# Performance work log

Measured on AMD Instinct MI355X. Metric: run time of the kernel, lower is better.

## Reference

```python
import jax, jax.numpy as jnp
import numpy as np

P, K, C = 16, 256, 3          # patches, boxes per patch, classes
PATCH = 1024                   # patch size (px)
SIZE_FACTOR = 1.0
IOU_T = 0.55                   # wbf_iou_thresh
PRE = P * K                    # pre_wbf_detections = 4096
POST = 1000                    # max_detections


def setup_inputs() -> dict:
    key = jax.random.key(0)
    k1, k2, k3, k4, k5, k6 = jax.random.split(key, 6)
    # realistic xyxy boxes inside a 1024px patch, 8..56 px wide
    cx = jax.random.uniform(k1, (P, K)) * (PATCH - 64)
    cy = jax.random.uniform(k2, (P, K)) * (PATCH - 64)
    w = jax.random.uniform(k3, (P, K)) * 48.0 + 8.0
    h = jax.random.uniform(k4, (P, K)) * 48.0 + 8.0
    b4 = jnp.stack([cx, cy, cx + w, cy + h], axis=-1)          # [P,K,4]
    scores = jax.random.uniform(k5, (P, K, 1))                  # (0,1)
    labels = jax.random.randint(k6, (P, K, 1), 0, C).astype(jnp.float32)
    boxes = jnp.concatenate([b4, scores, labels], axis=-1)      # [P,K,6]
    stride = float(int(PATCH * 0.8))
    grid = jnp.arange(4, dtype=jnp.float32) * stride
    ox = jnp.tile(grid, 4)
    oy = jnp.repeat(grid, 4)
    offsets = jnp.stack([ox, oy], axis=-1)                      # [P,2] (xmin,ymin)
    return {"boxes": boxes, "offsets": offsets}


def _wbf(dets):
    """Greedy class-aware weighted boxes fusion.

    dets: [N,6] = (x1,y1,x2,y2,score,label). Sequential scan: each box joins
    the first existing cluster of the SAME class with IoU(merged_box)>IOU_T,
    else opens a new cluster. Class-aware matching inside one scan is
    math-equivalent to the original per-class loops (clusters never mix
    classes; within-class order is preserved; output is score-sorted anyway).
    """
    N = dets.shape[0]
    init = (
        jnp.zeros((N, 4), jnp.float32),   # mbox: current merged box per slot
        jnp.zeros((N, 4), jnp.float32),   # wsum: sum(score*box)
        jnp.zeros((N,), jnp.float32),     # ssum: sum(score)
        jnp.zeros((N,), jnp.float32),     # cnt:  members per cluster
        jnp.full((N,), -1.0, jnp.float32),# cls:  cluster class id
        jnp.array(0, jnp.int32),          # num:  clusters opened so far
    )

    def step(carry, row):
        mbox, wsum, ssum, cnt, cls, num = carry
        box, score, label = row[:4], row[4], row[5]
        # IoU of `box` against every cluster slot (vectorized)
        xx1 = jnp.maximum(mbox[:, 0], box[0])
        yy1 = jnp.maximum(mbox[:, 1], box[1])
        xx2 = jnp.minimum(mbox[:, 2], box[2])
        yy2 = jnp.minimum(mbox[:, 3], box[3])
        inter = jnp.clip(xx2 - xx1, 0.0) * jnp.clip(yy2 - yy1, 0.0)
        area_a = (box[2] - box[0]) * (box[3] - box[1])
        area_b = (mbox[:, 2] - mbox[:, 0]) * (mbox[:, 3] - mbox[:, 1])
        union = area_a + area_b - inter
        iou = jnp.where(union > 0.0, inter / union, 0.0)
        match = (cnt > 0) & (cls == label) & (iou > IOU_T)
        has = jnp.any(match)
        idx = jnp.where(has, jnp.argmax(match).astype(jnp.int32), num)
        wsum = wsum.at[idx].add(score * box)
        ssum = ssum.at[idx].add(score)
        cnt = cnt.at[idx].add(1.0)
        mbox = mbox.at[idx].set(wsum[idx] / ssum[idx])
        cls = cls.at[idx].set(label)
        num = num + jnp.where(has, 0, 1).astype(jnp.int32)
        return (mbox, wsum, ssum, cnt, cls, num), None

    (mbox, wsum, ssum, cnt, cls, num), _ = jax.lax.scan(step, init, dets)
    valid = cnt > 0.0
    scores = jnp.where(valid, ssum / jnp.maximum(cnt, 1.0), 0.0)  # mean score
    return mbox, scores, cls, valid


def reference(boxes, offsets):
    # PatchMerger: shift boxes into global coords, rescale by size_factor
    off4 = jnp.concatenate([offsets, offsets], axis=-1)[:, None, :]  # [P,1,4]
    b4 = (boxes[..., :4] + off4) / SIZE_FACTOR                       # [P,K,4]
    dets = jnp.concatenate([b4, boxes[..., 4:]], axis=-1).reshape(-1, 6)[:PRE]
    # WBF clustering
    mbox, scores, cls, valid = _wbf(dets)
    # sort by score desc, keep top POST; pad rows zeroed
    sort_key = jnp.where(valid, scores, -1.0)
    topv, topi = jax.lax.top_k(sort_key, POST)
    out = jnp.concatenate([mbox, scores[:, None], cls[:, None]], axis=-1)[topi]
    out = jnp.where((topv >= 0.0)[:, None], out, 0.0)
    return out  # [POST, 6]
```

## Files before the change

### kernel.cpp

```cpp
#include <hip/hip_runtime.h>

#define N 4096
#define NT 1024
#define BATCH 64
#define KCAND 8
#define IOU_THR 0.55f
#define INF 0x7fffffff
#define NBINS 14
#define NBKT 42
#define BCAP 320

__device__ float4 g_wsum[N];

__device__ __forceinline__ float rl_f(float v, int lane) {
  return __int_as_float(__builtin_amdgcn_readlane(__float_as_int(v), lane));
}
__device__ __forceinline__ int rl_i(int v, int lane) {
  return __builtin_amdgcn_readlane(v, lane);
}

__global__ __launch_bounds__(NT) void wbf_kernel(
    const float* __restrict__ boxes,
    const float* __restrict__ offs,
    float* __restrict__ out)
{
  __shared__ float4 s_mbox[N];
  __shared__ float  s_ssum[N];
  __shared__ unsigned short s_cc[N];
  __shared__ unsigned short s_bkt[NBKT][BCAP];
  __shared__ int s_bktlen[NBKT];
  __shared__ unsigned long long s_dirty[64];
  __shared__ uint4 s_cand4[BATCH];
  __shared__ int   s_ccnt[BATCH];
  __shared__ float s_batch[BATCH][6];
  __shared__ unsigned s_bgate[BATCH];
  __shared__ unsigned long long s_pm[BATCH];
  __shared__ int s_min[2];
  __shared__ int s_num, s_resume, s_ovf;

  const int tid = threadIdx.x;

  if (tid < 64) s_dirty[tid] = 0ull;
  if (tid < NBKT) s_bktlen[tid] = 0;
  if (tid == 0) { s_num = 0; s_resume = BATCH; s_ovf = 0; s_min[0] = INF; s_min[1] = INF; }

  for (int t0 = 0; t0 < N; t0 += BATCH) {
    if (tid < BATCH * 6) {
      int b = tid / 6, f = tid % 6;
      int gi = t0 + b;
      float v = boxes[(size_t)gi * 6 + f];
      if (f < 4) v += offs[((gi >> 8) << 1) + (f & 1)];
      s_batch[b][f] = v;
    } else if (tid < BATCH * 7) {
      s_ccnt[tid - BATCH * 6] = 0;
    } else if (tid < BATCH * 8) {
      s_pm[tid - BATCH * 7] = 0ull;
    }
    __syncthreads();

    int nm0 = s_num;
    if (tid < BATCH) {
      int qx = (int)s_batch[tid][0];
      int qy = (int)s_batch[tid][1];
      int lb = (int)s_batch[tid][5];
      s_bgate[tid] = ((unsigned)((lb << 12) | qx) << 16) | (unsigned)qy;
    }
    __syncthreads();

    int use_linear = s_ovf;
    if (!use_linear) {
      int b = tid >> 4, sl = tid & 15;
      float qx1 = s_batch[b][0], qy1 = s_batch[b][1];
      float qx2 = s_batch[b][2], qy2 = s_batch[b][3];
      int cls = (int)s_batch[b][5];
      float aA = (qx2 - qx1) * (qy2 - qy1);
      int bb = ((int)qx1) >> 8;
      int jlo = bb > 0 ? bb - 1 : 0;
      int jhi = bb < NBINS - 1 ? bb + 1 : NBINS - 1;
      for (int j = jlo; j <= jhi; ++j) {
        int bk = cls * NBINS + j;
        int len = s_bktlen[bk]; if (len > BCAP) len = BCAP;
        for (int e = sl; e < len; e += 16) {
          int c = (int)s_bkt[bk][e];
          float4 m = s_mbox[c];
          if (fabsf(m.x - qx1) < 60.0f && fabsf(m.y - qy1) < 60.0f) {
            float xx1 = fmaxf(m.x, qx1), yy1 = fmaxf(m.y, qy1);
            float xx2 = fminf(m.z, qx2), yy2 = fminf(m.w, qy2);
            float iw = fmaxf(xx2 - xx1, 0.0f), ih = fmaxf(yy2 - yy1, 0.0f);
            float inter = iw * ih;
            float aB = (m.z - m.x) * (m.w - m.y);
            float uni = aA + aB - inter;
            if (uni > 0.0f && inter / uni > IOU_THR) {
              int pos = atomicAdd(&s_ccnt[b], 1);
              if (pos < KCAND) ((unsigned short*)&s_cand4[b])[pos] = (unsigned short)c;
            }
          }
        }
      }
    } else {
      for (int c = tid; c < nm0; c += NT) {
        float4 m = s_mbox[c];
        int mcls = (int)(s_cc[c] >> 14);
        float aB = (m.z - m.x) * (m.w - m.y);
        for (int b2 = 0; b2 < BATCH; ++b2) {
          float qx1 = s_batch[b2][0], qy1 = s_batch[b2][1];
          if (fabsf(m.x - qx1) < 60.0f && fabsf(m.y - qy1) < 60.0f &&
              mcls == (int)s_batch[b2][5]) {
            float qx2 = s_batch[b2][2], qy2 = s_batch[b2][3];
            float xx1 = fmaxf(m.x, qx1), yy1 = fmaxf(m.y, qy1);
            float xx2 = fminf(m.z, qx2), yy2 = fminf(m.w, qy2);
            float iw = fmaxf(xx2 - xx1, 0.0f), ih = fmaxf(yy2 - yy1, 0.0f);
            float inter = iw * ih;
            float aA = (qx2 - qx1) * (qy2 - qy1);
            float uni = aA + aB - inter;
            if (uni > 0.0f && inter / uni > IOU_THR) {
              int pos = atomicAdd(&s_ccnt[b2], 1);
              if (pos < KCAND) ((unsigned short*)&s_cand4[b2])[pos] = (unsigned short)c;
            }
          }
        }
      }
    }
    #pragma unroll
    for (int q = 0; q < 4; ++q) {
      int p = tid + q * NT;
      int bb2 = p >> 6, jj = p & 63;
      if (jj < bb2) {
        unsigned gb = s_bgate[bb2], gj = s_bgate[jj];
        unsigned dx = __usad(gb >> 16, gj >> 16, 0u);
        unsigned dy = __usad(gb & 0xFFFFu, gj & 0xFFFFu, 0u);
        if (dx <= 60u && dy <= 60u) {
          float ax1 = s_batch[bb2][0], ay1 = s_batch[bb2][1];
          float ax2 = s_batch[bb2][2], ay2 = s_batch[bb2][3];
          float jx1 = s_batch[jj][0], jy1 = s_batch[jj][1];
          float jx2 = s_batch[jj][2], jy2 = s_batch[jj][3];
          float xx1 = fmaxf(ax1, jx1), yy1 = fmaxf(ay1, jy1);
          float xx2 = fminf(ax2, jx2), yy2 = fminf(ay2, jy2);
          float iw = fmaxf(xx2 - xx1, 0.0f), ih = fmaxf(yy2 - yy1, 0.0f);
          float inter = iw * ih;
          float aA = (ax2 - ax1) * (ay2 - ay1);
          float aB = (jx2 - jx1) * (jy2 - jy1);
          float uni = aA + aB - inter;
          if (uni > 0.0f && inter / uni > IOU_THR)
            atomicOr(&s_pm[bb2], 1ull << jj);
        }
      }
    }
    __syncthreads();

    if (tid < 64) {
      const int lane = tid;
      float p0 = s_batch[lane][0], p1 = s_batch[lane][1], p2 = s_batch[lane][2];
      float p3 = s_batch[lane][3], p4 = s_batch[lane][4], p5 = s_batch[lane][5];
      int   cc_l = s_ccnt[lane];
      uint4 cp_l = s_cand4[lane];
      unsigned long long pm_l = s_pm[lane];
      int pml_lo = (int)(unsigned)pm_l, pml_hi = (int)(unsigned)(pm_l >> 32);
      int c0 = (int)(cp_l.x & 0xFFFFu);
      float4 wp0 = make_float4(0.f, 0.f, 0.f, 0.f);
      float ssp0 = 1.0f; int ctp0 = 0;
      if (cc_l > 0) { wp0 = g_wsum[c0]; ssp0 = s_ssum[c0]; ctp0 = (int)s_cc[c0]; }

      unsigned long long anycand = __ballot(cc_l > 0);
      unsigned long long OVF = __ballot(cc_l > KCAND);
      unsigned long long F = __ballot(cc_l > 0 || pm_l != 0ull);
      int rs = BATCH;
      if (OVF) rs = (int)__builtin_ctzll(OVF);
      unsigned long long lowrs = (rs >= 64) ? ~0ull : ((1ull << rs) - 1ull);
      unsigned long long rem = F & lowrs;
      unsigned long long NEWM = ~F & lowrs;
      unsigned long long consumed = 0ull;

      int nmod = 0;
      int e_valid = 0, e_idx = INF, e_ct = 0, e_origbb = -1;
      float e_cls = -1.0f;
      float e_m0=0,e_m1=0,e_m2=0,e_m3=0, e_w0=0,e_w1=0,e_w2=0,e_w3=0, e_ss=0;

      while (rem) {
        int b = (int)__builtin_ctzll(rem);
        rem &= rem - 1ull;
        float bx1 = rl_f(p0, b), by1 = rl_f(p1, b);
        float bx2 = rl_f(p2, b), by2 = rl_f(p3, b);
        float sc  = rl_f(p4, b), lbf = rl_f(p5, b);

        int v = INF;
        if (e_valid && e_cls == lbf &&
            fabsf(e_m0 - bx1) < 60.0f && fabsf(e_m1 - by1) < 60.0f) {
          float xx1 = fmaxf(e_m0, bx1), yy1 = fmaxf(e_m1, by1);
          float xx2 = fminf(e_m2, bx2), yy2 = fminf(e_m3, by2);
          float iw = fmaxf(xx2 - xx1, 0.0f), ih = fmaxf(yy2 - yy1, 0.0f);
          float inter = iw * ih;
          float aA = (bx2 - bx1) * (by2 - by1);
          float aB = (e_m2 - e_m0) * (e_m3 - e_m1);
          float uni = aA + aB - inter;
          if (uni > 0.0f && inter / uni > IOU_THR) v = e_idx;
        }
        if ((anycand >> b) & 1ull) {
          int cc = rl_i(cc_l, b);
          unsigned w0 = (unsigned)rl_i((int)cp_l.x, b);
          unsigned w1 = (unsigned)rl_i((int)cp_l.y, b);
          unsigned w2 = (unsigned)rl_i((int)cp_l.z, b);
          unsigned w3 = (unsigned)rl_i((int)cp_l.w, b);
          if (lane < cc) {
            unsigned w = (lane >= 6) ? w3 : (lane >= 4) ? w2 : (lane >= 2) ? w1 : w0;
            int ci = (int)((w >> ((lane & 1) * 16)) & 0xFFFFu);
            if (!((s_dirty[ci >> 6] >> (ci & 63)) & 1ull)) v = min(v, ci);
          }
        }
        unsigned long long ball = __ballot(v != INF);
        int mn = INF;
        if (ball != 0ull) {
          if (__popcll(ball) == 1) {
            mn = rl_i(v, (int)__builtin_ctzll(ball));
          } else {
            int t = v;
            for (int o = 32; o; o >>= 1) t = min(t, __shfl_xor(t, o));
            mn = t;
          }
        }
        unsigned long long pc =
            (((unsigned long long)(unsigned)rl_i(pml_hi, b)) << 32) |
            (unsigned long long)(unsigned)rl_i(pml_lo, b);
        pc &= ~F & ~consumed;
        int pj = 64, pairidx = INF;
        if (pc) {
          pj = (int)__builtin_ctzll(pc);
          pairidx = nm0 + (int)__builtin_popcountll(NEWM & ((1ull << pj) - 1ull));
        }
        if (pairidx < mn) mn = pairidx;

        if (mn == INF) {
          int nidx = nm0 + (int)__builtin_popcountll(NEWM & ((1ull << b) - 1ull));
          NEWM |= 1ull << b;
          if (lane == nmod) {
            e_valid = 1; e_idx = nidx; e_cls = lbf; e_origbb = -1;
            e_w0 = sc * bx1; e_w1 = sc * by1; e_w2 = sc * bx2; e_w3 = sc * by2;
            e_ss = sc; e_ct = 1;
            e_m0 = e_w0 / e_ss; e_m1 = e_w1 / e_ss; e_m2 = e_w2 / e_ss; e_m3 = e_w3 / e_ss;
          }
          nmod++;
        } else {
          bool mine = e_valid && (e_idx == mn);
          unsigned long long mb = __ballot(mine);
          int owner;
          if (mb != 0ull) {
            owner = (int)__builtin_ctzll(mb);
            if (mine) {
              e_w0 += sc * bx1; e_w1 += sc * by1; e_w2 += sc * bx2; e_w3 += sc * by2;
              e_ss += sc; e_ct += 1;
              e_m0 = e_w0 / e_ss; e_m1 = e_w1 / e_ss; e_m2 = e_w2 / e_ss; e_m3 = e_w3 / e_ss;
            }
          } else if (mn < nm0) {
            owner = nmod;
            int rc0 = rl_i(c0, b);
            if (lane == nmod) {
              float w0, w1, w2, w3, ss; int ctp;
              if (mn == rc0) {
                w0 = rl_f(wp0.x, b); w1 = rl_f(wp0.y, b);
                w2 = rl_f(wp0.z, b); w3 = rl_f(wp0.w, b);
                ss = rl_f(ssp0, b);  ctp = rl_i(ctp0, b);
              } else {
                float4 w = g_wsum[mn];
                w0 = w.x; w1 = w.y; w2 = w.z; w3 = w.w;
                ss = s_ssum[mn]; ctp = (int)s_cc[mn];
              }
              e_valid = 1; e_idx = mn; e_cls = lbf;
              e_origbb = ((int)(w0 / ss)) >> 8;
              e_w0 = w0 + sc * bx1; e_w1 = w1 + sc * by1;
              e_w2 = w2 + sc * bx2; e_w3 = w3 + sc * by2;
              e_ss = ss + sc; e_ct = (ctp & 0x3FFF) + 1;
              e_m0 = e_w0 / e_ss; e_m1 = e_w1 / e_ss; e_m2 = e_w2 / e_ss; e_m3 = e_w3 / e_ss;
              atomicOr(&s_dirty[mn >> 6], 1ull << (mn & 63));
            }
            nmod++;
          } else {
            owner = nmod;
            consumed |= 1ull << pj;
            if (lane == nmod) {
              float jx1 = rl_f(p0, pj), jy1 = rl_f(p1, pj);
              float jx2 = rl_f(p2, pj), jy2 = rl_f(p3, pj);
              float jsc = rl_f(p4, pj);
              e_valid = 1; e_idx = mn; e_cls = lbf; e_origbb = -1;
              e_w0 = jsc * jx1 + sc * bx1; e_w1 = jsc * jy1 + sc * by1;
              e_w2 = jsc * jx2 + sc * bx2; e_w3 = jsc * jy2 + sc * by2;
              e_ss = jsc + sc; e_ct = 2;
              e_m0 = e_w0 / e_ss; e_m1 = e_w1 / e_ss; e_m2 = e_w2 / e_ss; e_m3 = e_w3 / e_ss;
            }
            nmod++;
          }
          float nx1 = rl_f(e_m0, owner), ny1 = rl_f(e_m1, owner);
          float nx2 = rl_f(e_m2, owner), ny2 = rl_f(e_m3, owner);
          bool dp = false;
          if (p5 == lbf) {
            float xx1 = fmaxf(nx1, p0), yy1 = fmaxf(ny1, p1);
            float xx2 = fminf(nx2, p2), yy2 = fminf(ny2, p3);
            float iw = fmaxf(xx2 - xx1, 0.0f), ih = fmaxf(yy2 - yy1, 0.0f);
            float inter = iw * ih;
            float aA = (p2 - p0) * (p3 - p1);
            float aB = (nx2 - nx1) * (ny2 - ny1);
            float uni = aA + aB - inter;
            dp = (uni > 0.0f) && (inter / uni > IOU_THR);
          }
          unsigned long long det = __ballot(dp);
          unsigned long long himask = (b >= 63) ? 0ull : (~0ull << (b + 1));
          det &= ~F & ~consumed & lowrs & himask;
          if (det) { F |= det; rem |= det; NEWM &= ~det; }
        }
      }

      if (e_valid) {
        s_mbox[e_idx] = make_float4(e_m0, e_m1, e_m2, e_m3);
        g_wsum[e_idx] = make_float4(e_w0, e_w1, e_w2, e_w3);
        s_ssum[e_idx] = e_ss;
        s_cc[e_idx] = (unsigned short)(e_ct | (((int)e_cls) << 14));
        int nb = ((int)e_m0) >> 8;
        if (nb < 0) nb = 0; if (nb > NBINS - 1) nb = NBINS - 1;
        if (nb != e_origbb) {
          int bk = ((int)e_cls) * NBINS + nb;
          int p = atomicAdd(&s_bktlen[bk], 1);
          if (p < BCAP) s_bkt[bk][p] = (unsigned short)e_idx; else s_ovf = 1;
        }
      }
      {
        unsigned long long selfbit = 1ull << lane;
        if (NEWM & ~F & ~consumed & selfbit) {
          int idx = nm0 + (int)__builtin_popcountll(NEWM & (selfbit - 1ull));
          float w0 = p4 * p0, w1 = p4 * p1, w2 = p4 * p2, w3 = p4 * p3;
          float m0 = w0 / p4, m1 = w1 / p4, m2 = w2 / p4, m3 = w3 / p4;
          g_wsum[idx] = make_float4(w0, w1, w2, w3);
          s_ssum[idx] = p4;
          s_cc[idx] = (unsigned short)(1 | (((int)p5) << 14));
          s_mbox[idx] = make_float4(m0, m1, m2, m3);
          int nb = ((int)m0) >> 8;
          if (nb < 0) nb = 0; if (nb > NBINS - 1) nb = NBINS - 1;
          int bk = ((int)p5) * NBINS + nb;
          int p = atomicAdd(&s_bktlen[bk], 1);
          if (p < BCAP) s_bkt[bk][p] = (unsigned short)idx; else s_ovf = 1;
        }
      }
      s_dirty[lane] = 0ull;
      if (lane == 0) {
        s_num = nm0 + (int)__builtin_popcountll(NEWM);
        s_resume = rs;
      }
    }
    __syncthreads();

    int rs2 = s_resume;
    if (rs2 < BATCH) {
      for (int i = rs2; i < BATCH; ++i) {
        float bx1 = s_batch[i][0], by1 = s_batch[i][1];
        float bx2 = s_batch[i][2], by2 = s_batch[i][3];
        float sc  = s_batch[i][4];
        int lb = (int)s_batch[i][5];
        int nm = s_num;
        float aA = (bx2 - bx1) * (by2 - by1);
        int mymin = INF;
        for (int c = tid; c < nm; c += NT) {
          float4 m = s_mbox[c];
          if (fabsf(m.x - bx1) < 60.0f && fabsf(m.y - by1) < 60.0f &&
              (int)(s_cc[c] >> 14) == lb) {
            float xx1 = fmaxf(m.x, bx1), yy1 = fmaxf(m.y, by1);
            float xx2 = fminf(m.z, bx2), yy2 = fminf(m.w, by2);
            float iw = fmaxf(xx2 - xx1, 0.0f), ih = fmaxf(yy2 - yy1, 0.0f);
            float inter = iw * ih;
            float aB = (m.z - m.x) * (m.w - m.y);
            float uni = aA + aB - inter;
            if (uni > 0.0f && inter / uni > IOU_THR) mymin = min(mymin, c);
          }
        }
        if (mymin != INF) atomicMin(&s_min[i & 1], mymin);
        __syncthreads();
        int mn = s_min[i & 1];
        if (tid == 0) {
          s_min[(i + 1) & 1] = INF;
          bool has = (mn != INF);
          int idx = has ? mn : nm;
          float w0, w1, w2, w3, ss; int ct, ob = -1;
          if (has) {
            float4 w = g_wsum[idx];
            w0 = w.x; w1 = w.y; w2 = w.z; w3 = w.w;
            ss = s_ssum[idx]; ct = (int)(s_cc[idx] & 0x3FFF);
            ob = ((int)s_mbox[idx].x) >> 8;
          } else { w0 = w1 = w2 = w3 = 0.0f; ss = 0.0f; ct = 0; }
          w0 += sc * bx1; w1 += sc * by1; w2 += sc * bx2; w3 += sc * by2;
          ss += sc; ct += 1;
          float m0 = w0 / ss, m1 = w1 / ss, m2 = w2 / ss, m3 = w3 / ss;
          g_wsum[idx] = make_float4(w0, w1, w2, w3);
          s_ssum[idx] = ss;
          s_cc[idx] = (unsigned short)(ct | (lb << 14));
          s_mbox[idx] = make_float4(m0, m1, m2, m3);
          int nb = ((int)m0) >> 8;
          if (nb < 0) nb = 0; if (nb > NBINS - 1) nb = NBINS - 1;
          if (nb != ob) {
            int bk = lb * NBINS + nb;
            int p = atomicAdd(&s_bktlen[bk], 1);
            if (p < BCAP) s_bkt[bk][p] = (unsigned short)idx; else s_ovf = 1;
          }
          if (!has) s_num = nm + 1;
        }
        __syncthreads();
      }
      if (tid == 0) { s_min[0] = INF; s_min[1] = INF; }
    }
  }

  __syncthreads();
  unsigned long long* s_keys = (unsigned long long*)s_mbox;
  int num = s_num;
  for (int j = tid; j < N; j += NT) {
    unsigned int lo = ~(unsigned int)j;
    unsigned long long key;
    if (j < num) {
      float ct = (float)(s_cc[j] & 0x3FFF);
      float sco = s_ssum[j] / fmaxf(ct, 1.0f);
      unsigned int bb = __float_as_uint(sco) | 0x80000000u;
      key = ((unsigned long long)bb << 32) | lo;
    } else {
      key = (0x407FFFFFull << 32) | lo;
    }
    s_keys[j] = key;
  }
  __syncthreads();

  for (int k = 2; k <= N; k <<= 1) {
    for (int j = k >> 1; j > 0; j >>= 1) {
      #pragma unroll
      for (int w = 0; w < N / NT; ++w) {
        int a0 = tid + (w << 10);
        int l = a0 ^ j;
        if (l > a0) {
          unsigned long long a = s_keys[a0], bq = s_keys[l];
          bool desc = ((a0 & k) == 0);
          bool sw = desc ? (a < bq) : (a > bq);
          if (sw) { s_keys[a0] = bq; s_keys[l] = a; }
        }
      }
      __syncthreads();
    }
  }

  if (tid < 1000) {
    unsigned long long key = s_keys[tid];
    unsigned int hi = (unsigned int)(key >> 32);
    float* o = out + (size_t)tid * 6;
    if (hi & 0x80000000u) {
      int j = (int)(~(unsigned int)key);
      float4 w = g_wsum[j];
      float ss = s_ssum[j];
      o[0] = w.x / ss; o[1] = w.y / ss; o[2] = w.z / ss; o[3] = w.w / ss;
      o[4] = __uint_as_float(hi & 0x7FFFFFFFu);
      o[5] = (float)(s_cc[j] >> 14);
    } else {
      o[0] = 0.0f; o[1] = 0.0f; o[2] = 0.0f;
      o[3] = 0.0f; o[4] = 0.0f; o[5] = 0.0f;
    }
  }
}

extern "C" void kernel_launch(void* const* d_in, const int* in_sizes, int n_in,
                              void* d_out, int out_size, void* d_ws, size_t ws_size,
                              hipStream_t stream) {
  const float* boxes = (const float*)d_in[0];
  const float* offs  = (const float*)d_in[1];
  float* out = (float*)d_out;
  hipLaunchKernelGGL(wbf_kernel, dim3(1), dim3(NT), 0, stream, boxes, offs, out);
}
```

Before: 307.7 us.

## Double-buffer batches and prefetch next batch during serial wave-0 resolve

Batch staging arrays become double-buffered. While wave 0 runs the serial cluster-resolution loop for the current batch, wave 1 loads the next batch from global memory and builds its intra-batch pair-overlap mask with cross-lane readlanes. This moves the batch load, gate computation and pairwise IoU phase out of the critical path and removes one barrier per batch. It also changes the ownership-class check to use the owner's cluster class and adds an extra barrier on the fallback path, which could alter behaviour.

```diff
diff --git a/kernel.cpp b/kernel.cpp
--- a/kernel.cpp
+++ b/kernel.cpp
@@ -30,11 +30,11 @@
   __shared__ unsigned short s_bkt[NBKT][BCAP];
   __shared__ int s_bktlen[NBKT];
   __shared__ unsigned long long s_dirty[64];
-  __shared__ uint4 s_cand4[BATCH];
-  __shared__ int   s_ccnt[BATCH];
-  __shared__ float s_batch[BATCH][6];
-  __shared__ unsigned s_bgate[BATCH];
-  __shared__ unsigned long long s_pm[BATCH];
+  __shared__ uint4 s_cand4[2][BATCH];
+  __shared__ int   s_ccnt[2][BATCH];
+  __shared__ float s_batch[2][BATCH][6];
+  __shared__ unsigned s_bgate[2][BATCH];
+  __shared__ unsigned long long s_pm[2][BATCH];
   __shared__ int s_min[2];
   __shared__ int s_num, s_resume, s_ovf;
 
@@ -44,35 +44,56 @@
   if (tid < NBKT) s_bktlen[tid] = 0;
   if (tid == 0) { s_num = 0; s_resume = BATCH; s_ovf = 0; s_min[0] = INF; s_min[1] = INF; }
 
-  for (int t0 = 0; t0 < N; t0 += BATCH) {
-    if (tid < BATCH * 6) {
-      int b = tid / 6, f = tid % 6;
-      int gi = t0 + b;
-      float v = boxes[(size_t)gi * 6 + f];
-      if (f < 4) v += offs[((gi >> 8) << 1) + (f & 1)];
-      s_batch[b][f] = v;
-    } else if (tid < BATCH * 7) {
-      s_ccnt[tid - BATCH * 6] = 0;
-    } else if (tid < BATCH * 8) {
-      s_pm[tid - BATCH * 7] = 0ull;
-    }
-    __syncthreads();
-
+  if (tid < BATCH) {
+    const float* br = boxes + (size_t)tid * 6;
+    float ox = offs[0], oy = offs[1];
+    float x1 = br[0] + ox, y1 = br[1] + oy;
+    float x2 = br[2] + ox, y2 = br[3] + oy;
+    s_batch[0][tid][0] = x1; s_batch[0][tid][1] = y1;
+    s_batch[0][tid][2] = x2; s_batch[0][tid][3] = y2;
+    s_batch[0][tid][4] = br[4]; s_batch[0][tid][5] = br[5];
+    s_bgate[0][tid] = ((unsigned)(((int)br[5] << 12) | (int)x1) << 16) | (unsigned)(int)y1;
+    s_ccnt[0][tid] = 0;
+    s_pm[0][tid] = 0ull;
+  }
+  __syncthreads();
+  #pragma unroll
+  for (int q = 0; q < 4; ++q) {
+    int p = tid + q * NT;
+    int bb2 = p >> 6, jj = p & 63;
+    if (jj < bb2) {
+      unsigned gb = s_bgate[0][bb2], gj = s_bgate[0][jj];
+      unsigned dx = __usad(gb >> 16, gj >> 16, 0u);
+      unsigned dy = __usad(gb & 0xFFFFu, gj & 0xFFFFu, 0u);
+      if (dx <= 60u && dy <= 60u) {
+        float ax1 = s_batch[0][bb2][0], ay1 = s_batch[0][bb2][1];
+        float ax2 = s_batch[0][bb2][2], ay2 = s_batch[0][bb2][3];
+        float jx1 = s_batch[0][jj][0], jy1 = s_batch[0][jj][1];
+        float jx2 = s_batch[0][jj][2], jy2 = s_batch[0][jj][3];
+        float xx1 = fmaxf(ax1, jx1), yy1 = fmaxf(ay1, jy1);
+        float xx2 = fminf(ax2, jx2), yy2 = fminf(ay2, jy2);
+        float iw = fmaxf(xx2 - xx1, 0.0f), ih = fmaxf(yy2 - yy1, 0.0f);
+        float inter = iw * ih;
+        float aA = (ax2 - ax1) * (ay2 - ay1);
+        float aB = (jx2 - jx1) * (jy2 - jy1);
+        float uni = aA + aB - inter;
+        if (uni > 0.0f && inter / uni > IOU_THR)
+          atomicOr(&s_pm[0][bb2], 1ull << jj);
+      }
+    }
+  }
+  __syncthreads();
+
+  for (int t = 0; t < N / BATCH; ++t) {
+    int cur = t & 1, nxt = cur ^ 1;
     int nm0 = s_num;
-    if (tid < BATCH) {
-      int qx = (int)s_batch[tid][0];
-      int qy = (int)s_batch[tid][1];
-      int lb = (int)s_batch[tid][5];
-      s_bgate[tid] = ((unsigned)((lb << 12) | qx) << 16) | (unsigned)qy;
-    }
-    __syncthreads();
 
     int use_linear = s_ovf;
     if (!use_linear) {
       int b = tid >> 4, sl = tid & 15;
-      float qx1 = s_batch[b][0], qy1 = s_batch[b][1];
-      float qx2 = s_batch[b][2], qy2 = s_batch[b][3];
-      int cls = (int)s_batch[b][5];
+      float qx1 = s_batch[cur][b][0], qy1 = s_batch[cur][b][1];
+      float qx2 = s_batch[cur][b][2], qy2 = s_batch[cur][b][3];
+      int cls = (int)s_batch[cur][b][5];
       float aA = (qx2 - qx1) * (qy2 - qy1);
       int bb = ((int)qx1) >> 8;
       int jlo = bb > 0 ? bb - 1 : 0;
@@ -91,8 +112,8 @@
             float aB = (m.z - m.x) * (m.w - m.y);
             float uni = aA + aB - inter;
             if (uni > 0.0f && inter / uni > IOU_THR) {
-              int pos = atomicAdd(&s_ccnt[b], 1);
-              if (pos < KCAND) ((unsigned short*)&s_cand4[b])[pos] = (unsigned short)c;
+              int pos = atomicAdd(&s_ccnt[cur][b], 1);
+              if (pos < KCAND) ((unsigned short*)&s_cand4[cur][b])[pos] = (unsigned short)c;
             }
           }
         }
@@ -103,10 +124,10 @@
         int mcls = (int)(s_cc[c] >> 14);
         float aB = (m.z - m.x) * (m.w - m.y);
         for (int b2 = 0; b2 < BATCH; ++b2) {
-          float qx1 = s_batch[b2][0], qy1 = s_batch[b2][1];
+          float qx1 = s_batch[cur][b2][0], qy1 = s_batch[cur][b2][1];
           if (fabsf(m.x - qx1) < 60.0f && fabsf(m.y - qy1) < 60.0f &&
-              mcls == (int)s_batch[b2][5]) {
-            float qx2 = s_batch[b2][2], qy2 = s_batch[b2][3];
+              mcls == (int)s_batch[cur][b2][5]) {
+            float qx2 = s_batch[cur][b2][2], qy2 = s_batch[cur][b2][3];
             float xx1 = fmaxf(m.x, qx1), yy1 = fmaxf(m.y, qy1);
             float xx2 = fminf(m.z, qx2), yy2 = fminf(m.w, qy2);
             float iw = fmaxf(xx2 - xx1, 0.0f), ih = fmaxf(yy2 - yy1, 0.0f);
@@ -114,35 +135,10 @@
             float aA = (qx2 - qx1) * (qy2 - qy1);
             float uni = aA + aB - inter;
             if (uni > 0.0f && inter / uni > IOU_THR) {
-              int pos = atomicAdd(&s_ccnt[b2], 1);
-              if (pos < KCAND) ((unsigned short*)&s_cand4[b2])[pos] = (unsigned short)c;
+              int pos = atomicAdd(&s_ccnt[cur][b2], 1);
+              if (pos < KCAND) ((unsigned short*)&s_cand4[cur][b2])[pos] = (unsigned short)c;
             }
           }
-        }
-      }
-    }
-    #pragma unroll
-    for (int q = 0; q < 4; ++q) {
-      int p = tid + q * NT;
-      int bb2 = p >> 6, jj = p & 63;
-      if (jj < bb2) {
-        unsigned gb = s_bgate[bb2], gj = s_bgate[jj];
-        unsigned dx = __usad(gb >> 16, gj >> 16, 0u);
-        unsigned dy = __usad(gb & 0xFFFFu, gj & 0xFFFFu, 0u);
-        if (dx <= 60u && dy <= 60u) {
-          float ax1 = s_batch[bb2][0], ay1 = s_batch[bb2][1];
-          float ax2 = s_batch[bb2][2], ay2 = s_batch[bb2][3];
-          float jx1 = s_batch[jj][0], jy1 = s_batch[jj][1];
-          float jx2 = s_batch[jj][2], jy2 = s_batch[jj][3];
-          float xx1 = fmaxf(ax1, jx1), yy1 = fmaxf(ay1, jy1);
-          float xx2 = fminf(ax2, jx2), yy2 = fminf(ay2, jy2);
-          float iw = fmaxf(xx2 - xx1, 0.0f), ih = fmaxf(yy2 - yy1, 0.0f);
-          float inter = iw * ih;
-          float aA = (ax2 - ax1) * (ay2 - ay1);
-          float aB = (jx2 - jx1) * (jy2 - jy1);
-          float uni = aA + aB - inter;
-          if (uni > 0.0f && inter / uni > IOU_THR)
-            atomicOr(&s_pm[bb2], 1ull << jj);
         }
       }
     }
@@ -150,11 +146,11 @@
 
     if (tid < 64) {
       const int lane = tid;
-      float p0 = s_batch[lane][0], p1 = s_batch[lane][1], p2 = s_batch[lane][2];
-      float p3 = s_batch[lane][3], p4 = s_batch[lane][4], p5 = s_batch[lane][5];
-      int   cc_l = s_ccnt[lane];
-      uint4 cp_l = s_cand4[lane];
-      unsigned long long pm_l = s_pm[lane];
+      float p0 = s_batch[cur][lane][0], p1 = s_batch[cur][lane][1], p2 = s_batch[cur][lane][2];
+      float p3 = s_batch[cur][lane][3], p4 = s_batch[cur][lane][4], p5 = s_batch[cur][lane][5];
+      int   cc_l = s_ccnt[cur][lane];
+      uint4 cp_l = s_cand4[cur][lane];
+      unsigned long long pm_l = s_pm[cur][lane];
       int pml_lo = (int)(unsigned)pm_l, pml_hi = (int)(unsigned)(pm_l >> 32);
       int c0 = (int)(cp_l.x & 0xFFFFu);
       float4 wp0 = make_float4(0.f, 0.f, 0.f, 0.f);
@@ -163,7 +159,8 @@
 
       unsigned long long anycand = __ballot(cc_l > 0);
       unsigned long long OVF = __ballot(cc_l > KCAND);
-      unsigned long long F = __ballot(cc_l > 0 || pm_l != 0ull);
+      unsigned long long PAIRS = __ballot(pm_l != 0ull);
+      unsigned long long F = anycand | PAIRS;
       int rs = BATCH;
       if (OVF) rs = (int)__builtin_ctzll(OVF);
       unsigned long long lowrs = (rs >= 64) ? ~0ull : ((1ull << rs) - 1ull);
@@ -213,9 +210,9 @@
           if (__popcll(ball) == 1) {
             mn = rl_i(v, (int)__builtin_ctzll(ball));
           } else {
-            int t = v;
-            for (int o = 32; o; o >>= 1) t = min(t, __shfl_xor(t, o));
-            mn = t;
+            int tt = v;
+            for (int o = 32; o; o >>= 1) tt = min(tt, __shfl_xor(tt, o));
+            mn = tt;
           }
         }
         unsigned long long pc =
@@ -291,7 +288,7 @@
           float nx1 = rl_f(e_m0, owner), ny1 = rl_f(e_m1, owner);
           float nx2 = rl_f(e_m2, owner), ny2 = rl_f(e_m3, owner);
           bool dp = false;
-          if (p5 == lbf) {
+          if (p5 == rl_f(e_cls, owner)) {
             float xx1 = fmaxf(nx1, p0), yy1 = fmaxf(ny1, p1);
             float xx2 = fminf(nx2, p2), yy2 = fminf(ny2, p3);
             float iw = fmaxf(xx2 - xx1, 0.0f), ih = fmaxf(yy2 - yy1, 0.0f);
@@ -343,16 +340,53 @@
         s_num = nm0 + (int)__builtin_popcountll(NEWM);
         s_resume = rs;
       }
+    } else if (tid < 128) {
+      if (t + 1 < N / BATCH) {
+        int lane = tid - 64;
+        int gi = (t + 1) * BATCH + lane;
+        const float* br = boxes + (size_t)gi * 6;
+        int p = gi >> 8;
+        float ox = offs[2 * p], oy = offs[2 * p + 1];
+        float x1 = br[0] + ox, y1 = br[1] + oy;
+        float x2 = br[2] + ox, y2 = br[3] + oy;
+        float sc = br[4], lb = br[5];
+        s_batch[nxt][lane][0] = x1; s_batch[nxt][lane][1] = y1;
+        s_batch[nxt][lane][2] = x2; s_batch[nxt][lane][3] = y2;
+        s_batch[nxt][lane][4] = sc; s_batch[nxt][lane][5] = lb;
+        unsigned g = ((unsigned)(((int)lb << 12) | (int)x1) << 16) | (unsigned)(int)y1;
+        s_bgate[nxt][lane] = g;
+        unsigned long long pm = 0ull;
+        for (int j = 0; j < 63; ++j) {
+          unsigned gj = (unsigned)rl_i((int)g, j);
+          unsigned dx = __usad(g >> 16, gj >> 16, 0u);
+          unsigned dy = __usad(g & 0xFFFFu, gj & 0xFFFFu, 0u);
+          if (j < lane && dx <= 60u && dy <= 60u) {
+            float jx1 = rl_f(x1, j), jy1 = rl_f(y1, j);
+            float jx2 = rl_f(x2, j), jy2 = rl_f(y2, j);
+            float xx1 = fmaxf(x1, jx1), yy1 = fmaxf(y1, jy1);
+            float xx2 = fminf(x2, jx2), yy2 = fminf(y2, jy2);
+            float iw = fmaxf(xx2 - xx1, 0.0f), ih = fmaxf(yy2 - yy1, 0.0f);
+            float inter = iw * ih;
+            float aA = (x2 - x1) * (y2 - y1);
+            float aB = (jx2 - jx1) * (jy2 - jy1);
+            float uni = aA + aB - inter;
+            if (uni > 0.0f && inter / uni > IOU_THR) pm |= 1ull << j;
+          }
+        }
+        s_pm[nxt][lane] = pm;
+      }
+    } else if (tid < 192) {
+      if (t + 1 < N / BATCH) s_ccnt[nxt][tid - 128] = 0;
     }
     __syncthreads();
 
     int rs2 = s_resume;
     if (rs2 < BATCH) {
       for (int i = rs2; i < BATCH; ++i) {
-        float bx1 = s_batch[i][0], by1 = s_batch[i][1];
-        float bx2 = s_batch[i][2], by2 = s_batch[i][3];
-        float sc  = s_batch[i][4];
-        int lb = (int)s_batch[i][5];
+        float bx1 = s_batch[cur][i][0], by1 = s_batch[cur][i][1];
+        float bx2 = s_batch[cur][i][2], by2 = s_batch[cur][i][3];
+        float sc  = s_batch[cur][i][4];
+        int lb = (int)s_batch[cur][i][5];
         int nm = s_num;
         float aA = (bx2 - bx1) * (by2 - by1);
         int mymin = INF;
@@ -401,7 +435,8 @@
         }
         __syncthreads();
       }
-      if (tid == 0) { s_min[0] = INF; s_min[1] = INF; }
+      if (tid == 0) { s_min[0] = INF; s_min[1] = INF; s_resume = BATCH; }
+      __syncthreads();
     }
   }
 
```

New measurement: 558.4 us. 81.5% more time.
